# Kernel optimization log

Measured on AMD Instinct MI355X. Metric: run time of the kernel, lower is better.

## Reference

```python
import jax, jax.numpy as jnp
import numpy as np

J = 21        # joints per skeleton
DIM = 3       # cfg.dataset.dim
NH = 7        # node_hsize = 2*DIM + 1
H = 4         # cfg.model.gat_heads
HD = 64       # h_dim
ALPHA = 0.2   # cfg.model.gat_alpha (LeakyReLU slope)


def setup_inputs() -> dict:
    key = jax.random.key(0)
    k1, k2, k3, k4, k5 = jax.random.split(key, 5)
    inputs = jax.random.normal(k1, (16, 1024, J * NH), dtype=jnp.float32)
    starts = jnp.arange(8, dtype=jnp.int64) * 128
    seq_start_end = jnp.stack([starts, starts + 128], axis=1)  # [8,2], unused in forward
    # Xavier-ish scaled params
    W_heads = jax.random.normal(k2, (H, NH, HD), dtype=jnp.float32) * (1.414 / np.sqrt(NH + HD) * np.sqrt(6) / 1.732)
    a_heads = jax.random.normal(k3, (H, 2 * HD), dtype=jnp.float32) * 0.1
    W_out = jax.random.normal(k4, (H * HD, HD), dtype=jnp.float32) * 0.08
    a_out = jax.random.normal(k5, (2 * HD,), dtype=jnp.float32) * 0.1
    return {"inputs": inputs, "seq_start_end": seq_start_end,
            "W_heads": W_heads, "a_heads": a_heads,
            "W_out": W_out, "a_out": a_out}


def _gat_attend(h, a1, a2):
    # h: [..., J, D]; a1,a2: [..., D] broadcastable; FC graph -> no adj mask
    f1 = jnp.sum(h * a1[..., None, :], axis=-1)          # [..., J]
    f2 = jnp.sum(h * a2[..., None, :], axis=-1)          # [..., J]
    e = jax.nn.leaky_relu(f1[..., :, None] + f2[..., None, :], ALPHA)  # [..., J, J]
    attn = jax.nn.softmax(e, axis=-1)
    return jnp.matmul(attn, h)                           # [..., J, D]


def reference(inputs, seq_start_end, W_heads, a_heads, W_out, a_out):
    F_, P, _ = inputs.shape
    # rebuild per-node graph features: [offset(dim) | loc(dim) | S(1)] per joint
    off = inputs[..., : J * DIM].reshape(F_, P, J, DIM)
    loc = inputs[..., J * DIM: 2 * J * DIM].reshape(F_, P, J, DIM)
    S = inputs[..., 2 * J * DIM:].reshape(F_, P, J, 1)
    x = jnp.concatenate([off, loc, S], axis=-1)          # [F,P,J,NH]
    # multi-head GAT layer (concat=True -> elu)
    h = jnp.einsum('fpjn,hnd->fphjd', x, W_heads)        # [F,P,H,J,HD]
    a1 = a_heads[:, :HD]                                 # [H,HD]
    a2 = a_heads[:, HD:]
    hp = jax.nn.elu(_gat_attend(h, a1[None, None], a2[None, None]))  # [F,P,H,J,HD]
    xcat = jnp.transpose(hp, (0, 1, 3, 2, 4)).reshape(F_, P, J, H * HD)
    # output GAT layer (concat=False -> raw h_prime), then outer elu + log_softmax
    h2 = jnp.einsum('fpjn,nd->fpjd', xcat, W_out)        # [F,P,J,HD]
    hp2 = _gat_attend(h2, a_out[None, None, :HD], a_out[None, None, HD:])
    out = jax.nn.log_softmax(jax.nn.elu(hp2), axis=-1)   # log_softmax over feature dim
    return out.reshape(F_, P, J * HD)
```

## Files before the change

### kernel.cpp

```cpp
#include <hip/hip_runtime.h>
#include <hip/hip_bf16.h>
#include <math.h>

#define J   21
#define NH  7
#define H   4
#define HD  64
#define ALPHA 0.2f
#define LOG2E 1.44269504f

#define HPS  264
#define JPA  40
#define JPT  24
#define F12S 32
#define ROW2 68

#define LDS_FLOATS 6676

typedef __attribute__((ext_vector_type(8))) short short8;
typedef __attribute__((ext_vector_type(4))) float floatx4;
typedef __attribute__((ext_vector_type(4))) unsigned uintx4;

static __device__ __forceinline__ short f2bf(float f) {
    __hip_bfloat16 h = __float2bfloat16(f);
    return __builtin_bit_cast(short, h);
}
static __device__ __forceinline__ short hi16(float f) {
    return (short)(__builtin_bit_cast(unsigned, f) >> 16);
}
static __device__ __forceinline__ unsigned pack2hi(float lo, float hi) {
    return __builtin_amdgcn_perm(__builtin_bit_cast(unsigned, hi),
                                 __builtin_bit_cast(unsigned, lo), 0x07060302u);
}
static __device__ __forceinline__ float elu(float a) {
    return (a > 0.f) ? a : (__expf(a) - 1.f);
}

#if __has_builtin(__builtin_amdgcn_exp2f)
static __device__ __forceinline__ float exp2_fast(float x) { return __builtin_amdgcn_exp2f(x); }
#else
static __device__ __forceinline__ float exp2_fast(float x) { return exp2f(x); }
#endif
#if __has_builtin(__builtin_amdgcn_rcpf)
static __device__ __forceinline__ float rcp_fast(float x) { return __builtin_amdgcn_rcpf(x); }
#else
static __device__ __forceinline__ float rcp_fast(float x) { return 1.f / x; }
#endif

__global__ void preconv(const float* __restrict__ Wo, const float* __restrict__ Wh,
                        const float* __restrict__ ah, const float* __restrict__ ao,
                        short* __restrict__ ws) {
    int t = blockIdx.x * 256 + threadIdx.x;
    if (t < 16384) {
        int n = t >> 8, k = t & 255;
        ws[t] = f2bf(Wo[k * HD + n]);
    } else if (t < 18432) {
        int i = t - 16384;
        int hh = i >> 9, d = (i >> 3) & 63, n = i & 7;
        ws[t] = (n < 7) ? f2bf(Wh[(hh * NH + n) * HD + d]) : (short)0;
    } else if (t < 18496) {
        int i = t - 18432;
        int hh = i >> 4, s = (i >> 3) & 1, n = i & 7;
        float acc = 0.f;
        if (n < 7) {
            for (int d = 0; d < HD; d++)
                acc += Wh[(hh * NH + n) * HD + d] * ah[hh * 2 * HD + s * HD + d];
        }
        ((float*)(ws + 18432))[i] = acc * LOG2E;
    } else if (t < 18624) {
        int i = t - 18496;
        ((float*)(ws + 18560))[i] = ao[i] * LOG2E;
    }
}

__global__ __launch_bounds__(256, 6)
void gat_kernel(const float* __restrict__ inp,
                const short* __restrict__ ws,
                float* __restrict__ out)
{
    __shared__ __align__(16) float smem[LDS_FLOATS];
    short* hp_bf  = (short*)smem;
    float* f1o    = smem;
    float* f2o    = smem + 24;
    float* f1     = smem + 3344;
    float* f2     = smem + 3472;
    short* h_t    = (short*)(smem + 3600);
    float* h2     = smem + 3600;
    short* h2_t   = (short*)(smem + 5032);

    const short* WoT  = ws;
    const short* WhT  = ws + 16384;
    const float* whaF = (const float*)(ws + 18432);
    const float* aoS  = (const float*)(ws + 18560);

    const int t    = threadIdx.x;
    const int w    = t >> 6;
    const int lane = t & 63;
    const int quad = lane >> 4;
    const int col  = lane & 15;
    const int rc   = (16 + col < 21) ? (16 + col) : 21;

    const size_t pair = blockIdx.x;
    const float* ip = inp + pair * (size_t)(J * NH);

    float v = 0.f;
    if (t < J * NH) v = ip[t];
    if (t < 110) {
        floatx4 z4 = {0.f, 0.f, 0.f, 0.f};
        *(floatx4*)(smem + 2904 + 4 * t) = z4;
    } else if (t < 114) {
        smem[6672 + (t - 110)] = 0.f;
    } else if (t < 158) {
        int i = t - 114;
        int hh = i / 11, jj = i - hh * 11;
        f2[hh * F12S + 21 + jj] = -INFINITY;
    }
    __syncthreads();
    if (t < J * NH) {
        int j, k;
        if (t < 63)       { j = t / 3;        k = t % 3; }
        else if (t < 126) { j = (t - 63) / 3; k = 3 + (t - 63) % 3; }
        else              { j = t - 126;      k = 6; }
        ((short*)(smem + 2904))[j * JPA + k] = hi16(v);
        smem[t] = v;
    }
    __syncthreads();

    {
        const short* x_bf = (const short*)(smem + 2904);
        short8 xa0 = *(const short8*)(x_bf + col * JPA + quad * 8);
        short8 xa1 = *(const short8*)(x_bf + rc  * JPA + quad * 8);
        #pragma unroll
        for (int nt = 0; nt < 4; nt++) {
            short8 b = *(const short8*)(WhT + ((w * 64 + nt * 16 + col) << 3) + quad * 8);
            floatx4 z = {0.f, 0.f, 0.f, 0.f};
            floatx4 c0 = __builtin_amdgcn_mfma_f32_16x16x32_bf16(xa0, b, z, 0, 0, 0);
            floatx4 c1 = __builtin_amdgcn_mfma_f32_16x16x32_bf16(xa1, b, z, 0, 0, 0);
            short* colbase = h_t + (w * 64 + nt * 16 + col) * JPT;
            *(uint2*)(colbase + quad * 4) =
                make_uint2(pack2hi(c0[0], c0[1]), pack2hi(c0[2], c0[3]));
            if (quad == 0)
                *(uint2*)(colbase + 16) =
                    make_uint2(pack2hi(c1[0], c1[1]), pack2hi(c1[2], c1[3]));
            else if (quad == 1)
                *(uint2*)(colbase + 20) = make_uint2(pack2hi(c1[0], 0.f), 0u);
        }
        if (t < 84) {
            int hh = t / 21, j = t - hh * 21;
            const float* xr = smem;
            float x0 = xr[j*3+0], x1 = xr[j*3+1], x2 = xr[j*3+2];
            float x3 = xr[63+j*3+0], x4 = xr[63+j*3+1], x5 = xr[63+j*3+2];
            float x6 = xr[126+j];
            const float* wp = whaF + hh * 16;
            f1[hh * F12S + j] = x0*wp[0] + x1*wp[1] + x2*wp[2] + x3*wp[3]
                              + x4*wp[4] + x5*wp[5] + x6*wp[6];
            f2[hh * F12S + j] = x0*wp[8] + x1*wp[9] + x2*wp[10] + x3*wp[11]
                              + x4*wp[12] + x5*wp[13] + x6*wp[14];
        }
    }
    __syncthreads();

    {
        float4 fqa = *(const float4*)(f2 + w * F12S + quad * 8);
        float4 fqb = *(const float4*)(f2 + w * F12S + quad * 8 + 4);
        float fq[8] = {fqa.x, fqa.y, fqa.z, fqa.w, fqb.x, fqb.y, fqb.z, fqb.w};
        float fi0 = f1[w * F12S + col];
        const int am  = 16 + col;
        const int amc = (am < 21) ? am : 20;
        float fi1 = f1[w * F12S + amc];
        float e0[8], e1[8];
        float s0 = 0.f, s1 = 0.f;
        #pragma unroll
        for (int j = 0; j < 8; j++) {
            float a0 = fi0 + fq[j]; a0 = fmaxf(a0, ALPHA * a0);
            float a1 = fi1 + fq[j]; a1 = fmaxf(a1, ALPHA * a1);
            float x0 = exp2_fast(a0);
            float x1 = exp2_fast(a1);
            e0[j] = x0; e1[j] = x1; s0 += x0; s1 += x1;
        }
        s0 += __shfl_xor(s0, 16); s0 += __shfl_xor(s0, 32);
        s1 += __shfl_xor(s1, 16); s1 += __shfl_xor(s1, 32);
        float inv0 = rcp_fast(s0), inv1 = rcp_fast(s1);
        uintx4 ua0, ua1;
        #pragma unroll
        for (int jj = 0; jj < 4; jj++) {
            ua0[jj] = pack2hi(e0[2*jj] * inv0, e0[2*jj+1] * inv0);
            ua1[jj] = pack2hi(e1[2*jj] * inv1, e1[2*jj+1] * inv1);
        }
        short8 aa0 = __builtin_bit_cast(short8, ua0);
        short8 aa1 = __builtin_bit_cast(short8, ua1);

        #pragma unroll
        for (int mt = 0; mt < 4; mt++) {
            short8 a = *(const short8*)(h_t + (w * 64 + mt * 16 + col) * JPT + quad * 8);
            floatx4 z = {0.f, 0.f, 0.f, 0.f};
            floatx4 c0 = __builtin_amdgcn_mfma_f32_16x16x32_bf16(a, aa0, z, 0, 0, 0);
            floatx4 c1 = __builtin_amdgcn_mfma_f32_16x16x32_bf16(a, aa1, z, 0, 0, 0);
            short* dst0 = hp_bf + col * HPS + w * 64 + mt * 16 + quad * 4;
            *(uint2*)dst0 = make_uint2(pack2hi(elu(c0[0]), elu(c0[1])),
                                       pack2hi(elu(c0[2]), elu(c0[3])));
            if (am < 21) {
                short* dst1 = hp_bf + am * HPS + w * 64 + mt * 16 + quad * 4;
                *(uint2*)dst1 = make_uint2(pack2hi(elu(c1[0]), elu(c1[1])),
                                           pack2hi(elu(c1[2]), elu(c1[3])));
            } else if (am == 21) {
                *(uint2*)(hp_bf + 21 * HPS + w * 64 + mt * 16 + quad * 4) =
                    make_uint2(0u, 0u);
            }
        }
    }
    __syncthreads();

    {
        floatx4 d0 = {0,0,0,0}, d1 = {0,0,0,0};
        #pragma unroll
        for (int s = 0; s < 8; s++) {
            short8 a0 = *(const short8*)(hp_bf + col * HPS + s * 32 + quad * 8);
            short8 a1 = *(const short8*)(hp_bf + rc  * HPS + s * 32 + quad * 8);
            short8 b  = *(const short8*)(WoT + (w * 16 + col) * 256 + s * 32 + quad * 8);
            d0 = __builtin_amdgcn_mfma_f32_16x16x32_bf16(a0, b, d0, 0, 0, 0);
            d1 = __builtin_amdgcn_mfma_f32_16x16x32_bf16(a1, b, d1, 0, 0, 0);
        }
        const int c = w * 16 + col;
        #pragma unroll
        for (int r = 0; r < 4; r++) {
            h2[(quad * 4 + r) * ROW2 + c] = d0[r];
            int row1 = 16 + quad * 4 + r;
            if (row1 < J) h2[row1 * ROW2 + c] = d1[r];
        }
        short* cb = h2_t + c * JPT;
        *(uint2*)(cb + quad * 4) = make_uint2(pack2hi(d0[0], d0[1]), pack2hi(d0[2], d0[3]));
        if (quad == 0)
            *(uint2*)(cb + 16) = make_uint2(pack2hi(d1[0], d1[1]), pack2hi(d1[2], d1[3]));
        else if (quad == 1)
            *(uint2*)(cb + 20) = make_uint2(pack2hi(d1[0], 0.f), 0u);
    }
    __syncthreads();

    if (t < 4 * 2 * J) {
        int which = (t >= 4 * J) ? 1 : 0;
        int r2 = t - which * 4 * J;
        int j = r2 >> 2, seg = r2 & 3;
        const float4* hrow = (const float4*)(h2 + j * ROW2) + seg * 4;
        const float4* ap   = (const float4*)(aoS + which * HD) + seg * 4;
        float sacc = 0.f;
        #pragma unroll
        for (int k = 0; k < 4; k++) {
            float4 hv = hrow[k], av = ap[k];
            sacc += hv.x*av.x + hv.y*av.y + hv.z*av.z + hv.w*av.w;
        }
        sacc += __shfl_xor(sacc, 1);
        sacc += __shfl_xor(sacc, 2);
        if (seg == 0) {
            if (which == 0) f1o[j] = sacc; else f2o[j] = sacc;
        }
    } else if (t < 179) {
        f2o[21 + (t - 168)] = -INFINITY;
    }
    __syncthreads();

    {
        const int mt = w & 1;
        const int rh = w >> 1;
        const int arow = mt * 16 + col;
        const int ar = (arow < 21) ? arow : 20;

        float4 fqa = *(const float4*)(f2o + quad * 8);
        float4 fqb = *(const float4*)(f2o + quad * 8 + 4);
        float fq[8] = {fqa.x, fqa.y, fqa.z, fqa.w, fqb.x, fqb.y, fqb.z, fqb.w};
        float fi = f1o[ar];
        float ev[8];
        float ssum = 0.f;
        #pragma unroll
        for (int j = 0; j < 8; j++) {
            float e = fi + fq[j]; e = fmaxf(e, ALPHA * e);
            float x = exp2_fast(e);
            ev[j] = x; ssum += x;
        }
        ssum += __shfl_xor(ssum, 16); ssum += __shfl_xor(ssum, 32);
        float inv = rcp_fast(ssum);
        uintx4 ua;
        #pragma unroll
        for (int jj = 0; jj < 4; jj++)
            ua[jj] = pack2hi(ev[2*jj] * inv, ev[2*jj+1] * inv);
        short8 a = __builtin_bit_cast(short8, ua);

        floatx4 acc[4];
        #pragma unroll
        for (int nt = 0; nt < 4; nt++) {
            short8 b = *(const short8*)(h2_t + (nt * 16 + col) * JPT + quad * 8);
            floatx4 z = {0,0,0,0};
            acc[nt] = __builtin_amdgcn_mfma_f32_16x16x32_bf16(a, b, z, 0, 0, 0);
        }
        float* outp = out + pair * (size_t)(J * HD);
        #pragma unroll
        for (int rr = 0; rr < 2; rr++) {
            int r = rh * 2 + rr;
            int row = mt * 16 + quad * 4 + r;
            float v0 = elu(acc[0][r]), v1 = elu(acc[1][r]);
            float v2 = elu(acc[2][r]), v3 = elu(acc[3][r]);
            float s = __expf(v0) + __expf(v1) + __expf(v2) + __expf(v3);
            s += __shfl_xor(s, 1);
            s += __shfl_xor(s, 2);
            s += __shfl_xor(s, 4);
            s += __shfl_xor(s, 8);
            float ls = __logf(s);
            if (row < J) {
                outp[row * HD +      col] = v0 - ls;
                outp[row * HD + 16 + col] = v1 - ls;
                outp[row * HD + 32 + col] = v2 - ls;
                outp[row * HD + 48 + col] = v3 - ls;
            }
        }
    }
}

extern "C" void kernel_launch(void* const* d_in, const int* in_sizes, int n_in,
                              void* d_out, int out_size, void* d_ws, size_t ws_size,
                              hipStream_t stream) {
    const float* inp = (const float*)d_in[0];
    const float* Wh  = (const float*)d_in[2];
    const float* ah  = (const float*)d_in[3];
    const float* Wo  = (const float*)d_in[4];
    const float* ao  = (const float*)d_in[5];
    float* outp = (float*)d_out;
    short* ws   = (short*)d_ws;

    hipLaunchKernelGGL(preconv, dim3(73), dim3(256), 0, stream, Wo, Wh, ah, ao, ws);

    const int pairs = in_sizes[0] / (J * NH);
    hipLaunchKernelGGL(gat_kernel, dim3(pairs), dim3(256), 0, stream,
                       inp, (const short*)ws, outp);
}
```

Baseline: 203.5 us.

## Alias LDS regions per head to shrink shared memory and raise occupancy

Reorganizes shared memory so each wave's head-projection buffer is overwritten in place by its first-layer attention output. Each wave first loads its whole h tile into registers, then writes the ELU result into the same slot. The h2 buffers now alias that region, which adds a barrier before they are written. LDS per block drops from about 26.7KB to about 16KB and launch bounds go from 6 to 8 blocks per SIMD-group. The cost is the extra barrier and more register pressure from holding the four A fragments.

```diff
diff --git a/kernel.cpp b/kernel.cpp
--- a/kernel.cpp
+++ b/kernel.cpp
@@ -9,13 +9,14 @@
 #define ALPHA 0.2f
 #define LOG2E 1.44269504f
 
-#define HPS  264
 #define JPA  40
 #define JPT  24
+#define HPR  72
+#define HSLOT 1584
 #define F12S 32
 #define ROW2 68
 
-#define LDS_FLOATS 6676
+#define LDS_FLOATS 4012
 
 typedef __attribute__((ext_vector_type(8))) short short8;
 typedef __attribute__((ext_vector_type(4))) float floatx4;
@@ -73,20 +74,19 @@
     }
 }
 
-__global__ __launch_bounds__(256, 6)
+__global__ __launch_bounds__(256, 8)
 void gat_kernel(const float* __restrict__ inp,
                 const short* __restrict__ ws,
                 float* __restrict__ out)
 {
     __shared__ __align__(16) float smem[LDS_FLOATS];
-    short* hp_bf  = (short*)smem;
-    float* f1o    = smem;
-    float* f2o    = smem + 24;
-    float* f1     = smem + 3344;
-    float* f2     = smem + 3472;
-    short* h_t    = (short*)(smem + 3600);
-    float* h2     = smem + 3600;
-    short* h2_t   = (short*)(smem + 5032);
+    short* regA   = (short*)smem;
+    float* h2     = smem;
+    short* h2_t   = (short*)(smem + 1432);
+    float* f1o    = smem + 3168;
+    float* f2o    = smem + 3192;
+    float* f1     = smem + 3756;
+    float* f2     = smem + 3884;
 
     const short* WoT  = ws;
     const short* WhT  = ws + 16384;
@@ -107,11 +107,13 @@
     if (t < J * NH) v = ip[t];
     if (t < 110) {
         floatx4 z4 = {0.f, 0.f, 0.f, 0.f};
-        *(floatx4*)(smem + 2904 + 4 * t) = z4;
-    } else if (t < 114) {
-        smem[6672 + (t - 110)] = 0.f;
-    } else if (t < 158) {
-        int i = t - 114;
+        *(floatx4*)(smem + 3168 + 4 * t) = z4;
+    } else if (t < 126) {
+        int i = t - 110;
+        int hh = i >> 2;
+        smem[hh * (HSLOT / 2) + (1536 / 2) + (i & 3)] = 0.f;
+    } else if (t < 170) {
+        int i = t - 126;
         int hh = i / 11, jj = i - hh * 11;
         f2[hh * F12S + 21 + jj] = -INFINITY;
     }
@@ -121,13 +123,13 @@
         if (t < 63)       { j = t / 3;        k = t % 3; }
         else if (t < 126) { j = (t - 63) / 3; k = 3 + (t - 63) % 3; }
         else              { j = t - 126;      k = 6; }
-        ((short*)(smem + 2904))[j * JPA + k] = hi16(v);
-        smem[t] = v;
+        ((short*)(smem + 3168))[j * JPA + k] = hi16(v);
+        smem[3608 + t] = v;
     }
     __syncthreads();
 
     {
-        const short* x_bf = (const short*)(smem + 2904);
+        const short* x_bf = (const short*)(smem + 3168);
         short8 xa0 = *(const short8*)(x_bf + col * JPA + quad * 8);
         short8 xa1 = *(const short8*)(x_bf + rc  * JPA + quad * 8);
         #pragma unroll
@@ -136,7 +138,7 @@
             floatx4 z = {0.f, 0.f, 0.f, 0.f};
             floatx4 c0 = __builtin_amdgcn_mfma_f32_16x16x32_bf16(xa0, b, z, 0, 0, 0);
             floatx4 c1 = __builtin_amdgcn_mfma_f32_16x16x32_bf16(xa1, b, z, 0, 0, 0);
-            short* colbase = h_t + (w * 64 + nt * 16 + col) * JPT;
+            short* colbase = regA + w * HSLOT + (nt * 16 + col) * JPT;
             *(uint2*)(colbase + quad * 4) =
                 make_uint2(pack2hi(c0[0], c0[1]), pack2hi(c0[2], c0[3]));
             if (quad == 0)
@@ -147,7 +149,7 @@
         }
         if (t < 84) {
             int hh = t / 21, j = t - hh * 21;
-            const float* xr = smem;
+            const float* xr = smem + 3608;
             float x0 = xr[j*3+0], x1 = xr[j*3+1], x2 = xr[j*3+2];
             float x3 = xr[63+j*3+0], x4 = xr[63+j*3+1], x5 = xr[63+j*3+2];
             float x6 = xr[126+j];
@@ -190,22 +192,26 @@
         short8 aa0 = __builtin_bit_cast(short8, ua0);
         short8 aa1 = __builtin_bit_cast(short8, ua1);
 
+        short8 af[4];
+        #pragma unroll
+        for (int mt = 0; mt < 4; mt++)
+            af[mt] = *(const short8*)(regA + w * HSLOT + (mt * 16 + col) * JPT + quad * 8);
+
+        short* hb = regA + w * HSLOT;
         #pragma unroll
         for (int mt = 0; mt < 4; mt++) {
-            short8 a = *(const short8*)(h_t + (w * 64 + mt * 16 + col) * JPT + quad * 8);
             floatx4 z = {0.f, 0.f, 0.f, 0.f};
-            floatx4 c0 = __builtin_amdgcn_mfma_f32_16x16x32_bf16(a, aa0, z, 0, 0, 0);
-            floatx4 c1 = __builtin_amdgcn_mfma_f32_16x16x32_bf16(a, aa1, z, 0, 0, 0);
-            short* dst0 = hp_bf + col * HPS + w * 64 + mt * 16 + quad * 4;
+            floatx4 c0 = __builtin_amdgcn_mfma_f32_16x16x32_bf16(af[mt], aa0, z, 0, 0, 0);
+            floatx4 c1 = __builtin_amdgcn_mfma_f32_16x16x32_bf16(af[mt], aa1, z, 0, 0, 0);
+            short* dst0 = hb + col * HPR + mt * 16 + quad * 4;
             *(uint2*)dst0 = make_uint2(pack2hi(elu(c0[0]), elu(c0[1])),
                                        pack2hi(elu(c0[2]), elu(c0[3])));
             if (am < 21) {
-                short* dst1 = hp_bf + am * HPS + w * 64 + mt * 16 + quad * 4;
+                short* dst1 = hb + am * HPR + mt * 16 + quad * 4;
                 *(uint2*)dst1 = make_uint2(pack2hi(elu(c1[0]), elu(c1[1])),
                                            pack2hi(elu(c1[2]), elu(c1[3])));
             } else if (am == 21) {
-                *(uint2*)(hp_bf + 21 * HPS + w * 64 + mt * 16 + quad * 4) =
-                    make_uint2(0u, 0u);
+                *(uint2*)(hb + 21 * HPR + mt * 16 + quad * 4) = make_uint2(0u, 0u);
             }
         }
     }
@@ -215,12 +221,15 @@
         floatx4 d0 = {0,0,0,0}, d1 = {0,0,0,0};
         #pragma unroll
         for (int s = 0; s < 8; s++) {
-            short8 a0 = *(const short8*)(hp_bf + col * HPS + s * 32 + quad * 8);
-            short8 a1 = *(const short8*)(hp_bf + rc  * HPS + s * 32 + quad * 8);
+            const short* hb = regA + (s >> 1) * HSLOT;
+            const int f = (s & 1) * 32 + quad * 8;
+            short8 a0 = *(const short8*)(hb + col * HPR + f);
+            short8 a1 = *(const short8*)(hb + rc  * HPR + f);
             short8 b  = *(const short8*)(WoT + (w * 16 + col) * 256 + s * 32 + quad * 8);
             d0 = __builtin_amdgcn_mfma_f32_16x16x32_bf16(a0, b, d0, 0, 0, 0);
             d1 = __builtin_amdgcn_mfma_f32_16x16x32_bf16(a1, b, d1, 0, 0, 0);
         }
+        __syncthreads();
         const int c = w * 16 + col;
         #pragma unroll
         for (int r = 0; r < 4; r++) {
```

After: 197.6 us. 1.03x faster.
